# Kernel tuning notes

Hardware: AMD Instinct MI355X
Metric: run time of the kernel (lower is better)

## Reference

```python
import jax, jax.numpy as jnp
import numpy as np

K = 15
ALPHA = 5.0
PCT = 0.6
LAM_CLUSTER = 6.0
LAM_DIV = 0.1
MIN_CLUSTER_SIZE = 3
EPS_NORM = 1e-12
EPS_LOG = 1e-8


def setup_inputs() -> dict:
    key = jax.random.key(0)
    ks = jax.random.split(key, 7)
    B, D, C = 16384, 1024, 1000
    return {
        "fea_image": jax.random.normal(ks[0], (B, D), jnp.float32),
        "fea_ocr": jax.random.normal(ks[1], (B, D), jnp.float32),
        "fea_trans": jax.random.normal(ks[2], (B, D), jnp.float32),
        "cent_image": jax.random.normal(ks[3], (K, D), jnp.float32),
        "cent_ocr": jax.random.normal(ks[4], (K, D), jnp.float32),
        "cent_trans": jax.random.normal(ks[5], (K, D), jnp.float32),
        "out": jax.random.normal(ks[6], (B, C), jnp.float32),
    }


def _l2norm(x):
    # F.normalize(dim=1): divide by clamped L2 norm
    n = jnp.linalg.norm(x, axis=1, keepdims=True)
    return x / jnp.maximum(n, EPS_NORM)


def _attractive_loss(avg_sim):
    # avg_sim: [B]. kthvalue-based dynamic threshold (detached), sigmoid soft weighting.
    n = avg_sim.shape[0]
    num_keep = int(n * PCT)            # static (shape-derived)
    kth_idx = n - num_keep             # 0-based index of kth smallest (== kthvalue(k_th+1))
    thr = jnp.sort(jax.lax.stop_gradient(avg_sim))[kth_idx]
    w = jax.nn.sigmoid(ALPHA * (avg_sim - thr))
    return jnp.mean(w * (1.0 - avg_sim))


def _diversity_loss(assignments, probs):
    # Vectorized replacement of the per-cluster Python loop:
    # per-cluster mean softmax probs -> negative-entropy sum, gated by cluster size.
    sums = jax.ops.segment_sum(probs, assignments, num_segments=K)          # [K, C]
    counts = jax.ops.segment_sum(jnp.ones(assignments.shape, probs.dtype),
                                 assignments, num_segments=K)               # [K]
    mean_p = sums / jnp.maximum(counts, 1.0)[:, None]
    ent = jnp.sum(mean_p * jnp.log(mean_p + EPS_LOG), axis=-1)              # [K]
    valid = counts >= MIN_CLUSTER_SIZE
    return jnp.sum(jnp.where(valid, ent, 0.0))


def reference(fea_image, fea_ocr, fea_trans, cent_image, cent_ocr, cent_trans, out):
    # Cosine similarity of already-normalized vectors == dot product.
    sim_img = _l2norm(fea_image) @ _l2norm(cent_image).T     # [B, K]
    sim_ocr = _l2norm(fea_ocr) @ _l2norm(cent_ocr).T
    sim_trans = _l2norm(fea_trans) @ _l2norm(cent_trans).T

    total_attr = (_attractive_loss(sim_img.mean(axis=1))
                  + _attractive_loss(sim_ocr.mean(axis=1))
                  + _attractive_loss(sim_trans.mean(axis=1)))

    probs = jax.nn.softmax(out, axis=-1)                     # [B, C]
    assign_v = jnp.argmax(sim_img, axis=1)
    assign_t = jnp.argmax(sim_trans, axis=1)
    assign_a = jnp.argmax(sim_ocr, axis=1)

    total_div = (_diversity_loss(assign_v, probs)
                 + _diversity_loss(assign_t, probs)
                 + _diversity_loss(assign_a, probs))

    loss = LAM_CLUSTER * total_attr + LAM_DIV * total_div
    return out, loss
```

## Files before the change

kernel.cpp:

```cpp
#include <hip/hip_runtime.h>
#include <hip/hip_bf16.h>
#include <math.h>

#define B_ROWS 16384
#define DIM    1024
#define CLS    1000
#define KC     15

typedef __attribute__((ext_vector_type(8))) short short8;
typedef __attribute__((ext_vector_type(4))) float f32x4;

__device__ __forceinline__ unsigned short bf16rtn(float x) {
    unsigned u = __float_as_uint(x);
    unsigned r = (u + 0x7FFFu + ((u >> 16) & 1u)) >> 16;
    return (unsigned short)r;
}

__global__ __launch_bounds__(256) void k1_centnorm(const float* c0, const float* c1, const float* c2,
                                                   unsigned short* cnorm) {
    int bx = blockIdx.x;
    int m = bx >> 4, k = bx & 15;
    int t = threadIdx.x;
    unsigned short* outp = cnorm + ((m * 16 + k) << 10);
    if (k == 15) {
        outp[t * 4 + 0] = 0; outp[t * 4 + 1] = 0; outp[t * 4 + 2] = 0; outp[t * 4 + 3] = 0;
        return;
    }
    const float* src = (m == 0 ? c0 : (m == 1 ? c1 : c2)) + (k << 10);
    float4 f = ((const float4*)src)[t];
    float s = f.x * f.x + f.y * f.y + f.z * f.z + f.w * f.w;
    for (int d = 1; d < 64; d <<= 1) s += __shfl_xor(s, d);
    __shared__ float r4[4];
    int w = t >> 6, lane = t & 63;
    if (lane == 0) r4[w] = s;
    __syncthreads();
    float tot = r4[0] + r4[1] + r4[2] + r4[3];
    float inv = 1.0f / fmaxf(sqrtf(tot), 1e-12f);
    outp[t * 4 + 0] = bf16rtn(f.x * inv);
    outp[t * 4 + 1] = bf16rtn(f.y * inv);
    outp[t * 4 + 2] = bf16rtn(f.z * inv);
    outp[t * 4 + 3] = bf16rtn(f.w * inv);
}

__global__ __launch_bounds__(256) void k2_sim(const float* f0, const float* f1, const float* f2,
                                              const unsigned short* cnorm, float* avg, int* assign) {
    int t = threadIdx.x;
    int lane = t & 63, w = t >> 6;
    int wg = blockIdx.x * 4 + w;
    int m = wg >> 10;
    int tile = wg & 1023;
    int row_base = tile << 4;
    const float* fea = (m == 0 ? f0 : (m == 1 ? f1 : f2));

    int nrow = lane & 15;
    int k8 = (lane >> 4) << 3;
    const float* aptr = fea + (size_t)(row_base + nrow) * DIM + k8;
    const short8* bptr = (const short8*)(cnorm + ((m * 16 + nrow) << 10) + k8);

    f32x4 acc = {0.0f, 0.0f, 0.0f, 0.0f};
    float nacc = 0.0f;

#pragma unroll 8
    for (int s = 0; s < 32; ++s) {
        float4 a0 = *(const float4*)(aptr + s * 32);
        float4 a1 = *(const float4*)(aptr + s * 32 + 4);
        short8 bfr = bptr[s * 4];
        short8 afr;
        afr[0] = (short)bf16rtn(a0.x); afr[1] = (short)bf16rtn(a0.y);
        afr[2] = (short)bf16rtn(a0.z); afr[3] = (short)bf16rtn(a0.w);
        afr[4] = (short)bf16rtn(a1.x); afr[5] = (short)bf16rtn(a1.y);
        afr[6] = (short)bf16rtn(a1.z); afr[7] = (short)bf16rtn(a1.w);
        nacc = fmaf(a0.x, a0.x, nacc);
        nacc = fmaf(a0.y, a0.y, nacc);
        nacc = fmaf(a0.z, a0.z, nacc);
        nacc = fmaf(a0.w, a0.w, nacc);
        nacc = fmaf(a1.x, a1.x, nacc);
        nacc = fmaf(a1.y, a1.y, nacc);
        nacc = fmaf(a1.z, a1.z, nacc);
        nacc = fmaf(a1.w, a1.w, nacc);
        acc = __builtin_amdgcn_mfma_f32_16x16x32_bf16(afr, bfr, acc, 0, 0, 0);
    }

    float nsq = nacc;
    nsq += __shfl_xor(nsq, 16);
    nsq += __shfl_xor(nsq, 32);
    float inv = 1.0f / fmaxf(sqrtf(nsq), 1e-12f);

    int c = lane & 15;
    int quad = lane >> 4;
#pragma unroll
    for (int j = 0; j < 4; ++j) {
        int r = quad * 4 + j;
        float invr = __shfl(inv, r);
        float simv = acc[j] * invr;
        float sv = (c < 15) ? simv : 0.0f;
        float mv = (c < 15) ? simv : -INFINITY;
        int mi = c;
        for (int s = 1; s <= 8; s <<= 1) {
            sv += __shfl_xor(sv, s);
            float ov = __shfl_xor(mv, s);
            int oi = __shfl_xor(mi, s);
            bool take = (ov > mv) || (ov == mv && oi < mi);
            mv = take ? ov : mv;
            mi = take ? oi : mi;
        }
        if (c == 0) {
            int row = row_base + r;
            avg[m * B_ROWS + row] = sv * (1.0f / 15.0f);
            assign[m * B_ROWS + row] = mi;
        }
    }
}

__global__ __launch_bounds__(1024) void k3_select(const float* avg, float* attr_out) {
    int m = blockIdx.x;
    int t = threadIdx.x;
    const float* a = avg + m * B_ROWS;
    float av[16];
    unsigned kv[16];
#pragma unroll
    for (int i = 0; i < 16; ++i) {
        float x = a[i * 1024 + t];
        av[i] = x;
        unsigned u = __float_as_uint(x);
        kv[i] = (u & 0x80000000u) ? ~u : (u | 0x80000000u);
    }
    __shared__ unsigned sP, sR;
    __shared__ int ri[16];
    __shared__ float rf[16];
    if (t == 0) { sP = 0u; sR = 6554u; }
    __syncthreads();
    int w = t >> 6, lane = t & 63;
    for (int bit = 31; bit >= 0; --bit) {
        unsigned pref = sP;
        unsigned rr = sR;
        unsigned maskH = (bit == 31) ? 0u : (0xFFFFFFFFu << (bit + 1));
        int cnt = 0;
#pragma unroll
        for (int i = 0; i < 16; ++i) {
            bool match = (((kv[i] ^ pref) & maskH) == 0u);
            bool zero = (((kv[i] >> bit) & 1u) == 0u);
            cnt += (match && zero) ? 1 : 0;
        }
        for (int d = 1; d < 64; d <<= 1) cnt += __shfl_xor(cnt, d);
        if (lane == 0) ri[w] = cnt;
        __syncthreads();
        if (t == 0) {
            int c0 = 0;
            for (int i = 0; i < 16; ++i) c0 += ri[i];
            if ((int)rr >= c0) { sP = pref | (1u << bit); sR = rr - (unsigned)c0; }
        }
        __syncthreads();
    }
    unsigned key = sP;
    float thr = (key & 0x80000000u) ? __uint_as_float(key & 0x7FFFFFFFu)
                                    : __uint_as_float(~key);
    float s = 0.0f;
#pragma unroll
    for (int i = 0; i < 16; ++i) {
        float x = av[i];
        float wgt = 1.0f / (1.0f + __expf(-5.0f * (x - thr)));
        s += wgt * (1.0f - x);
    }
    for (int d = 1; d < 64; d <<= 1) s += __shfl_xor(s, d);
    if (lane == 0) rf[w] = s;
    __syncthreads();
    if (t == 0) {
        float tot = 0.0f;
        for (int i = 0; i < 16; ++i) tot += rf[i];
        attr_out[m] = tot / 16384.0f;
    }
}

__global__ __launch_bounds__(256) void k4_softprep(const float* out_in, float* out_copy, float* inv_denom) {
    int w = threadIdx.x >> 6, lane = threadIdx.x & 63;
    int row = blockIdx.x * 4 + w;
    const float4* src = (const float4*)(out_in + (size_t)row * CLS);
    float4* dst = (float4*)(out_copy + (size_t)row * CLS);
    float s = 0.0f;
#pragma unroll
    for (int i = 0; i < 4; ++i) {
        int idx = i * 64 + lane;
        if (idx < 250) {
            float4 v = src[idx];
            dst[idx] = v;
            s += __expf(v.x) + __expf(v.y) + __expf(v.z) + __expf(v.w);
        }
    }
    for (int d = 1; d < 64; d <<= 1) s += __shfl_xor(s, d);
    if (lane == 0) inv_denom[row] = 1.0f / s;
}

__device__ __forceinline__ void accsel(float (&a)[KC], int k, float p) {
    switch (k) {
    case 0:  a[0]  += p; break;
    case 1:  a[1]  += p; break;
    case 2:  a[2]  += p; break;
    case 3:  a[3]  += p; break;
    case 4:  a[4]  += p; break;
    case 5:  a[5]  += p; break;
    case 6:  a[6]  += p; break;
    case 7:  a[7]  += p; break;
    case 8:  a[8]  += p; break;
    case 9:  a[9]  += p; break;
    case 10: a[10] += p; break;
    case 11: a[11] += p; break;
    case 12: a[12] += p; break;
    case 13: a[13] += p; break;
    default: a[14] += p; break;
    }
}

__device__ __forceinline__ void phase_out(float (&acc)[KC], float* red, int slot, int cl, int t, float* dst) {
#pragma unroll
    for (int s = 0; s < 4; ++s) {
        if (slot == s) {
#pragma unroll
            for (int k = 0; k < KC; ++k) {
                if (s == 0) red[k * 256 + cl] = acc[k];
                else        red[k * 256 + cl] += acc[k];
            }
        }
        __syncthreads();
    }
    for (int i = t; i < KC * 250; i += 1024) {
        dst[i] = red[(i / 250) * 256 + (i % 250)];
    }
    __syncthreads();
}

__global__ __launch_bounds__(1024) void k5_seg(const float* out_in, const float* inv_denom,
                                               const int* assign, float* partials) {
    int t = threadIdx.x;
    int slot = t >> 8;
    int cl = t & 255;
    int q = blockIdx.y;
    bool active = (cl < 250);
    int colbase = q * 250 + cl;

    float a0acc[KC], a1acc[KC], a2acc[KC];
#pragma unroll
    for (int k = 0; k < KC; ++k) { a0acc[k] = 0.0f; a1acc[k] = 0.0f; a2acc[k] = 0.0f; }

    for (int row = blockIdx.x * 4 + slot; row < B_ROWS; row += 256) {
        float p = 0.0f;
        if (active) p = __expf(out_in[(size_t)row * CLS + colbase]) * inv_denom[row];
        int a0 = assign[row];
        int a1 = assign[B_ROWS + row];
        int a2 = assign[2 * B_ROWS + row];
        accsel(a0acc, a0, p);
        accsel(a1acc, a1, p);
        accsel(a2acc, a2, p);
    }

    __shared__ float red[KC * 256];
    float* dst = partials + (size_t)(blockIdx.y * 64 + blockIdx.x) * (3 * KC * 250);
    phase_out(a0acc, red, slot, cl, t, dst);
    phase_out(a1acc, red, slot, cl, t, dst + KC * 250);
    phase_out(a2acc, red, slot, cl, t, dst + 2 * KC * 250);
}

__global__ __launch_bounds__(256) void k6_entropy(const int* assign, const float* partials,
                                                  float* ent_out) {
    int bx = blockIdx.x;
    int m = bx / KC, k = bx % KC;
    int t = threadIdx.x;
    int w = t >> 6, lane = t & 63;
    int cnt = 0;
    for (int e = t; e < B_ROWS; e += 256) cnt += (assign[m * B_ROWS + e] == k) ? 1 : 0;
    for (int d = 1; d < 64; d <<= 1) cnt += __shfl_xor(cnt, d);
    __shared__ int ri[4];
    __shared__ float rf[4];
    if (lane == 0) ri[w] = cnt;
    __syncthreads();
    int count = ri[0] + ri[1] + ri[2] + ri[3];
    float denom = fmaxf((float)count, 1.0f);
    float es = 0.0f;
    for (int c = t; c < CLS; c += 256) {
        int cg = c / 250, cl = c % 250;
        float s = 0.0f;
        for (int b = 0; b < 64; ++b) {
            s += partials[(size_t)(cg * 64 + b) * (3 * KC * 250) + (m * KC + k) * 250 + cl];
        }
        float mp = s / denom;
        es += mp * __logf(mp + 1e-8f);
    }
    for (int d = 1; d < 64; d <<= 1) es += __shfl_xor(es, d);
    if (lane == 0) rf[w] = es;
    __syncthreads();
    if (t == 0) {
        float ent = rf[0] + rf[1] + rf[2] + rf[3];
        ent_out[m * KC + k] = (count >= 3) ? ent : 0.0f;
    }
}

__global__ __launch_bounds__(64) void k7_final(const float* attr, const float* ent, float* out_loss) {
    int t = threadIdx.x;
    float v = 0.0f;
    if (t < 45) v = 0.1f * ent[t];
    else if (t < 48) v = 6.0f * attr[t - 45];
    for (int d = 1; d < 64; d <<= 1) v += __shfl_xor(v, d);
    if (t == 0) out_loss[0] = v;
}

extern "C" void kernel_launch(void* const* d_in, const int* in_sizes, int n_in,
                              void* d_out, int out_size, void* d_ws, size_t ws_size,
                              hipStream_t stream) {
    const float* fi = (const float*)d_in[0];
    const float* fo = (const float*)d_in[1];
    const float* ft = (const float*)d_in[2];
    const float* ci = (const float*)d_in[3];
    const float* co = (const float*)d_in[4];
    const float* ct = (const float*)d_in[5];
    const float* outin = (const float*)d_in[6];
    float* dout = (float*)d_out;
    char* ws = (char*)d_ws;

    unsigned short* cnorm = (unsigned short*)(ws + 0);
    float* avg   = (float*)(ws + 98304);
    int* assign  = (int*)(ws + 294912);
    float* invd  = (float*)(ws + 491520);
    float* attr  = (float*)(ws + 557056);
    float* ent   = (float*)(ws + 557312);
    float* partials = (float*)(ws + 557568);

    hipLaunchKernelGGL(k1_centnorm, dim3(48), dim3(256), 0, stream, ci, co, ct, cnorm);
    hipLaunchKernelGGL(k2_sim, dim3(768), dim3(256), 0, stream, fi, fo, ft, cnorm, avg, assign);
    hipLaunchKernelGGL(k3_select, dim3(3), dim3(1024), 0, stream, avg, attr);
    hipLaunchKernelGGL(k4_softprep, dim3(4096), dim3(256), 0, stream, outin, dout, invd);
    hipLaunchKernelGGL(k5_seg, dim3(64, 4), dim3(1024), 0, stream, outin, invd, assign, partials);
    hipLaunchKernelGGL(k6_entropy, dim3(45), dim3(256), 0, stream, assign, partials, ent);
    hipLaunchKernelGGL(k7_final, dim3(1), dim3(64), 0, stream, attr, ent, dout + 16384000);
}
```

Baseline: 419.1 us.

## Use LDS atomics for segment sums and split partial reduction into parallel kernel

The per-thread 45-register switch-based accumulators in the segment-sum kernel are replaced with LDS atomicAdd into a shared 3x15x256 table. This removes the register pressure, the serial switch dispatch and the staged four-slot reduction. The 64-way reduction over block partials moves out of the 45-block entropy kernel into a separate, wider reduce kernel, which adds one launch. The sums buffer reuses the avg workspace region, which k3 has already consumed by that point. LDS atomics may contend when many rows share a cluster.

```diff
diff --git a/kernel.cpp b/kernel.cpp
--- a/kernel.cpp
+++ b/kernel.cpp
@@ -191,44 +191,6 @@
     if (lane == 0) inv_denom[row] = 1.0f / s;
 }
 
-__device__ __forceinline__ void accsel(float (&a)[KC], int k, float p) {
-    switch (k) {
-    case 0:  a[0]  += p; break;
-    case 1:  a[1]  += p; break;
-    case 2:  a[2]  += p; break;
-    case 3:  a[3]  += p; break;
-    case 4:  a[4]  += p; break;
-    case 5:  a[5]  += p; break;
-    case 6:  a[6]  += p; break;
-    case 7:  a[7]  += p; break;
-    case 8:  a[8]  += p; break;
-    case 9:  a[9]  += p; break;
-    case 10: a[10] += p; break;
-    case 11: a[11] += p; break;
-    case 12: a[12] += p; break;
-    case 13: a[13] += p; break;
-    default: a[14] += p; break;
-    }
-}
-
-__device__ __forceinline__ void phase_out(float (&acc)[KC], float* red, int slot, int cl, int t, float* dst) {
-#pragma unroll
-    for (int s = 0; s < 4; ++s) {
-        if (slot == s) {
-#pragma unroll
-            for (int k = 0; k < KC; ++k) {
-                if (s == 0) red[k * 256 + cl] = acc[k];
-                else        red[k * 256 + cl] += acc[k];
-            }
-        }
-        __syncthreads();
-    }
-    for (int i = t; i < KC * 250; i += 1024) {
-        dst[i] = red[(i / 250) * 256 + (i % 250)];
-    }
-    __syncthreads();
-}
-
 __global__ __launch_bounds__(1024) void k5_seg(const float* out_in, const float* inv_denom,
                                                const int* assign, float* partials) {
     int t = threadIdx.x;
@@ -238,30 +200,44 @@
     bool active = (cl < 250);
     int colbase = q * 250 + cl;
 
-    float a0acc[KC], a1acc[KC], a2acc[KC];
-#pragma unroll
-    for (int k = 0; k < KC; ++k) { a0acc[k] = 0.0f; a1acc[k] = 0.0f; a2acc[k] = 0.0f; }
+    __shared__ float red[3 * KC * 256];
+    for (int i = t; i < 3 * KC * 256; i += 1024) red[i] = 0.0f;
+    __syncthreads();
 
     for (int row = blockIdx.x * 4 + slot; row < B_ROWS; row += 256) {
-        float p = 0.0f;
-        if (active) p = __expf(out_in[(size_t)row * CLS + colbase]) * inv_denom[row];
         int a0 = assign[row];
         int a1 = assign[B_ROWS + row];
         int a2 = assign[2 * B_ROWS + row];
-        accsel(a0acc, a0, p);
-        accsel(a1acc, a1, p);
-        accsel(a2acc, a2, p);
-    }
-
-    __shared__ float red[KC * 256];
+        if (active) {
+            float p = __expf(out_in[(size_t)row * CLS + colbase]) * inv_denom[row];
+            atomicAdd(&red[a0 * 256 + cl], p);
+            atomicAdd(&red[(KC + a1) * 256 + cl], p);
+            atomicAdd(&red[(2 * KC + a2) * 256 + cl], p);
+        }
+    }
+    __syncthreads();
+
     float* dst = partials + (size_t)(blockIdx.y * 64 + blockIdx.x) * (3 * KC * 250);
-    phase_out(a0acc, red, slot, cl, t, dst);
-    phase_out(a1acc, red, slot, cl, t, dst + KC * 250);
-    phase_out(a2acc, red, slot, cl, t, dst + 2 * KC * 250);
-}
-
-__global__ __launch_bounds__(256) void k6_entropy(const int* assign, const float* partials,
-                                                  float* ent_out) {
+    for (int i = t; i < 3 * KC * 250; i += 1024) {
+        dst[i] = red[(i / 250) * 256 + (i % 250)];
+    }
+}
+
+__global__ __launch_bounds__(256) void k6a_reduce(const float* partials, float* sums) {
+    int i = blockIdx.x * 256 + threadIdx.x;
+    if (i >= 4 * 3 * KC * 250) return;
+    int q = i / (3 * KC * 250);
+    int j = i - q * (3 * KC * 250);
+    const float* p = partials + (size_t)q * 64 * (3 * KC * 250) + j;
+    float s = 0.0f;
+#pragma unroll 4
+    for (int b = 0; b < 64; ++b)
+        s += p[(size_t)b * (3 * KC * 250)];
+    sums[i] = s;
+}
+
+__global__ __launch_bounds__(256) void k6b_entropy(const int* assign, const float* sums,
+                                                   float* ent_out) {
     int bx = blockIdx.x;
     int m = bx / KC, k = bx % KC;
     int t = threadIdx.x;
@@ -277,11 +253,8 @@
     float denom = fmaxf((float)count, 1.0f);
     float es = 0.0f;
     for (int c = t; c < CLS; c += 256) {
-        int cg = c / 250, cl = c % 250;
-        float s = 0.0f;
-        for (int b = 0; b < 64; ++b) {
-            s += partials[(size_t)(cg * 64 + b) * (3 * KC * 250) + (m * KC + k) * 250 + cl];
-        }
+        int q = c / 250, cl = c % 250;
+        float s = sums[q * (3 * KC * 250) + (m * KC + k) * 250 + cl];
         float mp = s / denom;
         es += mp * __logf(mp + 1e-8f);
     }
@@ -323,12 +296,14 @@
     float* attr  = (float*)(ws + 557056);
     float* ent   = (float*)(ws + 557312);
     float* partials = (float*)(ws + 557568);
+    float* sums  = (float*)(ws + 98304);
 
     hipLaunchKernelGGL(k1_centnorm, dim3(48), dim3(256), 0, stream, ci, co, ct, cnorm);
     hipLaunchKernelGGL(k2_sim, dim3(768), dim3(256), 0, stream, fi, fo, ft, cnorm, avg, assign);
     hipLaunchKernelGGL(k3_select, dim3(3), dim3(1024), 0, stream, avg, attr);
     hipLaunchKernelGGL(k4_softprep, dim3(4096), dim3(256), 0, stream, outin, dout, invd);
     hipLaunchKernelGGL(k5_seg, dim3(64, 4), dim3(1024), 0, stream, outin, invd, assign, partials);
-    hipLaunchKernelGGL(k6_entropy, dim3(45), dim3(256), 0, stream, assign, partials, ent);
+    hipLaunchKernelGGL(k6a_reduce, dim3(176), dim3(256), 0, stream, partials, sums);
+    hipLaunchKernelGGL(k6b_entropy, dim3(45), dim3(256), 0, stream, assign, sums, ent);
     hipLaunchKernelGGL(k7_final, dim3(1), dim3(64), 0, stream, attr, ent, dout + 16384000);
 }
```

Measured after the change: 575.7 us. +37.4%, slower.
